# Optimization experiments

Measured on AMD Instinct MI355X. Metric: run time of the kernel, lower is better.

Reference implementation:

```python
import jax, jax.numpy as jnp
import numpy as np

R = 4  # num_relations


def rgcn_conv(x, src, dst, etype, W, root, bias):
    """PyG RGCNConv (aggr='mean', no self-loops):
    out_i = x_i @ root + bias + sum_r mean_{j in N_r(i)} (x_j @ W_r)
    x: [N,D], W: [R,D,H], root: [D,H], bias: [H]
    """
    N = x.shape[0]
    Rr, _, H = W.shape
    x_r = jnp.einsum('nd,rdh->rnh', x, W)          # [R,N,H] relation-transformed feats
    msg = x_r[etype, src]                          # [E,H] per-edge messages
    seg = etype * N + dst                          # combined (relation, dst) segment id
    sums = jax.ops.segment_sum(msg, seg, num_segments=Rr * N)            # [R*N,H]
    cnt = jax.ops.segment_sum(jnp.ones(msg.shape[0], msg.dtype), seg,
                              num_segments=Rr * N)                        # [R*N]
    mean = sums / jnp.maximum(cnt, 1.0)[:, None]
    agg = mean.reshape(Rr, N, H).sum(0)            # sum over relations
    return agg + x @ root + bias


def setup_inputs() -> dict:
    key = jax.random.key(0)
    ks = jax.random.split(key, 12)
    N, E, D, H, ED = 20000, 320000, 256, 256, 64
    s = lambda fan: 1.0 / np.sqrt(fan)
    return {
        'x': jax.random.normal(ks[0], (N, D), jnp.float32),
        'edge_index': jax.random.randint(ks[1], (2, E), 0, N),
        'edge_type': jax.random.randint(ks[2], (E,), 0, R),
        'edge_attr': jax.random.normal(ks[3], (E, ED), jnp.float32),
        'W0': jax.random.normal(ks[4], (R, D, H), jnp.float32) * s(D),
        'root0': jax.random.normal(ks[5], (D, H), jnp.float32) * s(D),
        'b0': jnp.zeros((H,), jnp.float32),
        'W1': jax.random.normal(ks[6], (R, H, H), jnp.float32) * s(H),
        'root1': jax.random.normal(ks[7], (H, H), jnp.float32) * s(H),
        'b1': jnp.zeros((H,), jnp.float32),
        'lin_w': jax.random.normal(ks[8], (H, 2), jnp.float32) * s(H),
        'lin_b': jnp.zeros((2,), jnp.float32),
    }


def reference(x, edge_index, edge_type, edge_attr, W0, root0, b0, W1, root1, b1, lin_w, lin_b):
    src, dst = edge_index[0], edge_index[1]
    h = jax.nn.relu(rgcn_conv(x, src, dst, edge_type, W0, root0, b0))
    h = rgcn_conv(h, src, dst, edge_type, W1, root1, b1)
    g = h.sum(axis=0, keepdims=True)   # global_add_pool, single graph -> [1,H]
    # dropout inactive in eval mode
    return g @ lin_w + lin_b           # [1,2]
```

## Files before the change

kernel.cpp:

```cpp
#include <hip/hip_runtime.h>
#include <hip/hip_bf16.h>

#define RREL 4
#define DIM 256
#define KDIM 1280
#define KMEAN 1024
#define BCAP 32

__device__ __forceinline__ float bf2f(unsigned short u) {
    union { unsigned int i; float f; } z; z.i = ((unsigned int)u) << 16; return z.f;
}
__device__ __forceinline__ unsigned short f2bf(float f) {
    __hip_bfloat16 h = __float2bfloat16(f);
    return *(unsigned short*)&h;
}

typedef __attribute__((ext_vector_type(8))) short bf16x8;
typedef __attribute__((ext_vector_type(8))) unsigned short u16x8;
typedef __attribute__((ext_vector_type(4))) float f32x4;


__global__ __launch_bounds__(256)
void prep(const int* __restrict__ etype, const int* __restrict__ src,
          const int* __restrict__ dst,
          int* __restrict__ counts, int* __restrict__ bucket, int N, int E,
          const float* __restrict__ x, __hip_bfloat16* __restrict__ xb, int n4,
          const float* __restrict__ W0, const float* __restrict__ root0,
          const float* __restrict__ W1, const float* __restrict__ root1,
          __hip_bfloat16* __restrict__ WT,
          int eb, int cb) {
    int b = blockIdx.x;
    if (b < eb) {
        int e = b * 256 + threadIdx.x;
        if (e < E) {
            int seg = etype[e] * N + dst[e];
            int p = atomicAdd(&counts[seg], 1);
            if (p < BCAP) bucket[(size_t)seg * BCAP + p] = src[e];
        }
    } else if (b < eb + cb) {
        int i = (b - eb) * 256 + threadIdx.x;
        if (i < n4) {
            float4 v = ((const float4*)x)[i];
            ushort4 u = make_ushort4(f2bf(v.x), f2bf(v.y), f2bf(v.z), f2bf(v.w));
            ((ushort4*)xb)[i] = u;
        }
    } else {
        __shared__ float tile[32][33];
        int q = b - eb - cb;
        int layer = q / 320; q -= layer * 320;
        int nblk = q / 40;
        int kblk = q - nblk * 40;
        const float* Wm = layer ? W1 : W0;
        const float* Rm = layer ? root1 : root0;
        int k0 = kblk * 32, n0 = nblk * 32;
        int tx = threadIdx.x & 31, ty = threadIdx.x >> 5;
        const float* srcp;
        int kbase;
        if (k0 < RREL * DIM) { srcp = Wm; kbase = k0; } else { srcp = Rm; kbase = k0 - RREL * DIM; }
#pragma unroll
        for (int j = 0; j < 4; j++) {
            int k = kbase + ty + j * 8;
            tile[ty + j * 8][tx] = srcp[(size_t)k * DIM + n0 + tx];
        }
        __syncthreads();
#pragma unroll
        for (int j = 0; j < 4; j++) {
            int n = n0 + ty + j * 8;
            WT[((size_t)layer * DIM + n) * KDIM + k0 + tx] = __float2bfloat16(tile[tx][ty + j * 8]);
        }
    }
}


__global__ __launch_bounds__(256)
void aggregate(const __hip_bfloat16* __restrict__ feat, const int* __restrict__ counts,
               const int* __restrict__ bucket, __hip_bfloat16* __restrict__ Y, int N) {
    int r = threadIdx.x >> 6, lane = threadIdx.x & 63;
    int h = lane >> 5, li = lane & 31;
    int i = blockIdx.x * 2 + h;
    if (i >= N) return;
    int seg = r * N + i;
    int cnt = min(counts[seg], BCAP);
    const unsigned short* fu = (const unsigned short*)feat;
    const int* bk = bucket + (size_t)seg * BCAP;
    float a[8] = {};
    for (int k = 0; k < cnt; k += 4) {
        int4 q = *(const int4*)(bk + k);
        float m1 = (k + 1 < cnt) ? 1.f : 0.f;
        float m2 = (k + 2 < cnt) ? 1.f : 0.f;
        float m3 = (k + 3 < cnt) ? 1.f : 0.f;
        int i0 = q.x;
        int i1 = m1 ? q.y : q.x;
        int i2 = m2 ? q.z : q.x;
        int i3 = m3 ? q.w : q.x;
        u16x8 v0 = *(const u16x8*)(fu + (size_t)i0 * DIM + li * 8);
        u16x8 v1 = *(const u16x8*)(fu + (size_t)i1 * DIM + li * 8);
        u16x8 v2 = *(const u16x8*)(fu + (size_t)i2 * DIM + li * 8);
        u16x8 v3 = *(const u16x8*)(fu + (size_t)i3 * DIM + li * 8);
#pragma unroll
        for (int j = 0; j < 8; j++)
            a[j] += bf2f(v0[j]) + m1 * bf2f(v1[j]) + m2 * bf2f(v2[j]) + m3 * bf2f(v3[j]);
    }
    float inv = (cnt > 0) ? 1.f / (float)cnt : 0.f;
    u16x8 u;
#pragma unroll
    for (int j = 0; j < 8; j++) u[j] = f2bf(a[j] * inv);
    *(u16x8*)((unsigned short*)Y + (size_t)i * KMEAN + r * DIM + li * 8) = u;
}


#define BMg 64
#define BKg 64

template <int MODE>
__global__ __launch_bounds__(256)
void gemm_mfma(const __hip_bfloat16* __restrict__ A,
               const __hip_bfloat16* __restrict__ Aself,
               const __hip_bfloat16* __restrict__ Bt,
               const float* __restrict__ bias,
               unsigned short* __restrict__ Cbf,
               float* __restrict__ gsum,
               int Nrows) {
    __shared__ short As[2][BMg * BKg];
    __shared__ short Bs[2][DIM * BKg];
    int t = threadIdx.x;
    int lane = t & 63;
    int w = t >> 6;
    size_t row0 = (size_t)blockIdx.x * BMg;

    const unsigned short* Ag = (const unsigned short*)A;
    const unsigned short* Sg = (const unsigned short*)Aself;
    const unsigned short* Bg = (const unsigned short*)Bt;

    float bb[4];
#pragma unroll
    for (int ni = 0; ni < 4; ni++) bb[ni] = bias[w * 64 + ni * 16 + (lane & 15)];

    f32x4 acc[4][4] = {};

    auto issue_tile = [&](int k0, short* as, short* bs) {
        const unsigned short* Abase;
        int kk, stride;
        if (k0 < KMEAN) { Abase = Ag; kk = k0; stride = KMEAN; }
        else            { Abase = Sg; kk = k0 - KMEAN; stride = DIM; }
#pragma unroll
        for (int h = 0; h < 2; h++) {
            int c = t + h * 256;
            int r = c >> 3, pl = c & 7, pg = pl ^ (r & 7);
            const unsigned short* ga = Abase + (row0 + r) * stride + kk + pg * 8;
            __builtin_amdgcn_global_load_lds(
                (const __attribute__((address_space(1))) void*)ga,
                (__attribute__((address_space(3))) void*)((char*)as + c * 16),
                16, 0, 0);
        }
#pragma unroll
        for (int h = 0; h < 8; h++) {
            int c = t + h * 256;
            int r = c >> 3, pl = c & 7, pg = pl ^ (r & 7);
            const unsigned short* gb = Bg + (size_t)r * KDIM + k0 + pg * 8;
            __builtin_amdgcn_global_load_lds(
                (const __attribute__((address_space(1))) void*)gb,
                (__attribute__((address_space(3))) void*)((char*)bs + c * 16),
                16, 0, 0);
        }
    };

    issue_tile(0, As[0], Bs[0]);
    int cur = 0;
    for (int k0 = 0; k0 < KDIM; k0 += BKg) {
        __syncthreads();
        if (k0 + BKg < KDIM) issue_tile(k0 + BKg, As[cur ^ 1], Bs[cur ^ 1]);
        const short* as = As[cur];
        const short* bs = Bs[cur];
#pragma unroll
        for (int ks = 0; ks < 2; ks++) {
            int p = ks * 4 + (lane >> 4);
            bf16x8 af[4], bfr[4];
#pragma unroll
            for (int mi = 0; mi < 4; mi++) {
                int m = mi * 16 + (lane & 15);
                af[mi] = *(const bf16x8*)&as[m * 64 + (p ^ (m & 7)) * 8];
            }
#pragma unroll
            for (int ni = 0; ni < 4; ni++) {
                int n = w * 64 + ni * 16 + (lane & 15);
                bfr[ni] = *(const bf16x8*)&bs[n * 64 + (p ^ (n & 7)) * 8];
            }
#pragma unroll
            for (int mi = 0; mi < 4; mi++)
#pragma unroll
                for (int ni = 0; ni < 4; ni++)
                    acc[mi][ni] = __builtin_amdgcn_mfma_f32_16x16x32_bf16(af[mi], bfr[ni], acc[mi][ni], 0, 0, 0);
        }
        cur ^= 1;
    }

    if (MODE == 0) {
#pragma unroll
        for (int mi = 0; mi < 4; mi++) {
#pragma unroll
            for (int j = 0; j < 4; j++) {
                size_t row = row0 + mi * 16 + (lane >> 4) * 4 + j;
                if (row < (size_t)Nrows) {
#pragma unroll
                    for (int ni = 0; ni < 4; ni++) {
                        size_t col = w * 64 + ni * 16 + (lane & 15);
                        float v = fmaxf(acc[mi][ni][j] + bb[ni], 0.f);
                        Cbf[row * DIM + col] = f2bf(v);
                    }
                }
            }
        }
    } else {
        float cs[4] = {};
#pragma unroll
        for (int ni = 0; ni < 4; ni++) {
#pragma unroll
            for (int mi = 0; mi < 4; mi++)
#pragma unroll
                for (int j = 0; j < 4; j++) {
                    size_t row = row0 + mi * 16 + (lane >> 4) * 4 + j;
                    if (row < (size_t)Nrows) cs[ni] += acc[mi][ni][j] + bb[ni];
                }
            cs[ni] += __shfl_xor(cs[ni], 16, 64);
            cs[ni] += __shfl_xor(cs[ni], 32, 64);
        }
        if (lane < 16) {
#pragma unroll
            for (int ni = 0; ni < 4; ni++)
                atomicAdd(&gsum[w * 64 + ni * 16 + lane], cs[ni]);
        }
    }
}


__global__ void final_lin(const float* __restrict__ g, const float* __restrict__ lw,
                          const float* __restrict__ lb, float* __restrict__ out) {
    __shared__ float s0[256], s1[256];
    int t = threadIdx.x;
    float gv = g[t];
    s0[t] = gv * lw[t * 2 + 0];
    s1[t] = gv * lw[t * 2 + 1];
    __syncthreads();
    for (int off = 128; off > 0; off >>= 1) {
        if (t < off) { s0[t] += s0[t + off]; s1[t] += s1[t + off]; }
        __syncthreads();
    }
    if (t == 0) { out[0] = s0[0] + lb[0]; out[1] = s1[0] + lb[1]; }
}


static inline char* align_up(char* p, size_t a) {
    return (char*)(((uintptr_t)p + (a - 1)) & ~(uintptr_t)(a - 1));
}

extern "C" void kernel_launch(void* const* d_in, const int* in_sizes, int n_in,
                              void* d_out, int out_size, void* d_ws, size_t ws_size,
                              hipStream_t stream) {
    const float* x     = (const float*)d_in[0];
    const int*   eidx  = (const int*)d_in[1];
    const int*   etype = (const int*)d_in[2];
    const float* W0    = (const float*)d_in[4];
    const float* root0 = (const float*)d_in[5];
    const float* b0    = (const float*)d_in[6];
    const float* W1    = (const float*)d_in[7];
    const float* root1 = (const float*)d_in[8];
    const float* b1    = (const float*)d_in[9];
    const float* lin_w = (const float*)d_in[10];
    const float* lin_b = (const float*)d_in[11];
    float* out = (float*)d_out;

    const int N = in_sizes[0] / DIM;
    const int E = in_sizes[2];
    const int RN = RREL * N;
    const int* src = eidx;
    const int* dst = eidx + E;

    const int gx = (N + BMg - 1) / BMg;
    const int Mpad = gx * BMg;

    char* w = (char*)d_ws;
    int* counts  = (int*)w; w += (size_t)RN * 4;
    float* g     = (float*)w; w += 256 * 4;
    size_t zero_bytes = (size_t)RN * 4 + 1024;
    int* bucket  = (int*)w; w += (size_t)RN * BCAP * 4;
    w = align_up(w, 16);
    __hip_bfloat16* WT = (__hip_bfloat16*)w; w += (size_t)2 * DIM * KDIM * 2;
    w = align_up(w, 16);
    __hip_bfloat16* Y  = (__hip_bfloat16*)w; w += (size_t)Mpad * KMEAN * 2;
    __hip_bfloat16* xb = (__hip_bfloat16*)w; w += (size_t)Mpad * DIM * 2;
    __hip_bfloat16* h1 = (__hip_bfloat16*)w; w += (size_t)Mpad * DIM * 2;

    hipMemsetAsync(counts, 0, zero_bytes, stream);

    int eb = (E + 255) / 256;
    int n4 = N * DIM / 4;
    int cb = (n4 + 255) / 256;
    int wb = (KDIM / 32) * (DIM / 32) * 2;

    prep<<<eb + cb + wb, 256, 0, stream>>>(etype, src, dst, counts, bucket, N, E,
                                           x, xb, n4,
                                           W0, root0, W1, root1, WT, eb, cb);

    int ab = (N + 1) / 2;
    aggregate<<<ab, 256, 0, stream>>>(xb, counts, bucket, Y, N);
    gemm_mfma<0><<<gx, 256, 0, stream>>>(Y, xb, WT, b0, (unsigned short*)h1, nullptr, N);
    aggregate<<<ab, 256, 0, stream>>>(h1, counts, bucket, Y, N);
    gemm_mfma<1><<<gx, 256, 0, stream>>>(Y, h1, WT + (size_t)DIM * KDIM, b1, nullptr, g, N);

    final_lin<<<1, 256, 0, stream>>>(g, lin_w, lin_b, out);
}
```

Measured before the change: 273.4 us.

## Collapse second RGCN layer into weighted column sums plus a GEMV

Because the second layer output is only sum-pooled, the layer is linear in h1. The sum over nodes can therefore be rewritten as per-source weighted column sums of h1, with weights 1/cnt accumulated per edge and relation, followed by a small GEMV with W1 and root1. This drops the second aggregation pass and the second big GEMM, as well as the W1 transpose and convert. It adds an edge-wise atomic scatter into wsr and float atomics in the column-sum kernel, which changes summation order. It also computes the second layer in fp32 from bf16 h1, and it uses the uncapped counts for the weights, whereas the kept aggregation path truncates buckets at BCAP.

Measured after the change: 270.6 us. No clear change (-1.0%).

```diff
diff --git a/kernel.cpp b/kernel.cpp
--- a/kernel.cpp
+++ b/kernel.cpp
@@ -18,6 +18,7 @@
 typedef __attribute__((ext_vector_type(8))) short bf16x8;
 typedef __attribute__((ext_vector_type(8))) unsigned short u16x8;
 typedef __attribute__((ext_vector_type(4))) float f32x4;
+typedef __attribute__((ext_vector_type(4))) float fx4;
 
 
 __global__ __launch_bounds__(256)
@@ -26,7 +27,6 @@
           int* __restrict__ counts, int* __restrict__ bucket, int N, int E,
           const float* __restrict__ x, __hip_bfloat16* __restrict__ xb, int n4,
           const float* __restrict__ W0, const float* __restrict__ root0,
-          const float* __restrict__ W1, const float* __restrict__ root1,
           __hip_bfloat16* __restrict__ WT,
           int eb, int cb) {
     int b = blockIdx.x;
@@ -40,23 +40,20 @@
     } else if (b < eb + cb) {
         int i = (b - eb) * 256 + threadIdx.x;
         if (i < n4) {
-            float4 v = ((const float4*)x)[i];
+            fx4 v = *((const fx4*)x + i);
             ushort4 u = make_ushort4(f2bf(v.x), f2bf(v.y), f2bf(v.z), f2bf(v.w));
             ((ushort4*)xb)[i] = u;
         }
     } else {
         __shared__ float tile[32][33];
         int q = b - eb - cb;
-        int layer = q / 320; q -= layer * 320;
         int nblk = q / 40;
         int kblk = q - nblk * 40;
-        const float* Wm = layer ? W1 : W0;
-        const float* Rm = layer ? root1 : root0;
         int k0 = kblk * 32, n0 = nblk * 32;
         int tx = threadIdx.x & 31, ty = threadIdx.x >> 5;
         const float* srcp;
         int kbase;
-        if (k0 < RREL * DIM) { srcp = Wm; kbase = k0; } else { srcp = Rm; kbase = k0 - RREL * DIM; }
+        if (k0 < RREL * DIM) { srcp = W0; kbase = k0; } else { srcp = root0; kbase = k0 - RREL * DIM; }
 #pragma unroll
         for (int j = 0; j < 4; j++) {
             int k = kbase + ty + j * 8;
@@ -66,7 +63,7 @@
 #pragma unroll
         for (int j = 0; j < 4; j++) {
             int n = n0 + ty + j * 8;
-            WT[((size_t)layer * DIM + n) * KDIM + k0 + tx] = __float2bfloat16(tile[tx][ty + j * 8]);
+            WT[(size_t)n * KDIM + k0 + tx] = __float2bfloat16(tile[tx][ty + j * 8]);
         }
     }
 }
@@ -74,7 +71,19 @@
 
 __global__ __launch_bounds__(256)
 void aggregate(const __hip_bfloat16* __restrict__ feat, const int* __restrict__ counts,
-               const int* __restrict__ bucket, __hip_bfloat16* __restrict__ Y, int N) {
+               const int* __restrict__ bucket, __hip_bfloat16* __restrict__ Y, int N,
+               const int* __restrict__ etype, const int* __restrict__ srcv,
+               const int* __restrict__ dstv, float* __restrict__ wsr, int E, int ab) {
+    if ((int)blockIdx.x >= ab) {
+        int e = (blockIdx.x - ab) * 256 + threadIdx.x;
+        if (e < E) {
+            int r = etype[e];
+            int seg = r * N + dstv[e];
+            float sc = 1.f / (float)counts[seg];
+            atomicAdd(&wsr[(size_t)srcv[e] * RREL + r], sc);
+        }
+        return;
+    }
     int r = threadIdx.x >> 6, lane = threadIdx.x & 63;
     int h = lane >> 5, li = lane & 31;
     int i = blockIdx.x * 2 + h;
@@ -112,14 +121,12 @@
 #define BMg 64
 #define BKg 64
 
-template <int MODE>
 __global__ __launch_bounds__(256)
 void gemm_mfma(const __hip_bfloat16* __restrict__ A,
                const __hip_bfloat16* __restrict__ Aself,
                const __hip_bfloat16* __restrict__ Bt,
                const float* __restrict__ bias,
                unsigned short* __restrict__ Cbf,
-               float* __restrict__ gsum,
                int Nrows) {
     __shared__ short As[2][BMg * BKg];
     __shared__ short Bs[2][DIM * BKg];
@@ -195,42 +202,62 @@
         cur ^= 1;
     }
 
-    if (MODE == 0) {
-#pragma unroll
-        for (int mi = 0; mi < 4; mi++) {
-#pragma unroll
-            for (int j = 0; j < 4; j++) {
-                size_t row = row0 + mi * 16 + (lane >> 4) * 4 + j;
-                if (row < (size_t)Nrows) {
-#pragma unroll
-                    for (int ni = 0; ni < 4; ni++) {
-                        size_t col = w * 64 + ni * 16 + (lane & 15);
-                        float v = fmaxf(acc[mi][ni][j] + bb[ni], 0.f);
-                        Cbf[row * DIM + col] = f2bf(v);
-                    }
+#pragma unroll
+    for (int mi = 0; mi < 4; mi++) {
+#pragma unroll
+        for (int j = 0; j < 4; j++) {
+            size_t row = row0 + mi * 16 + (lane >> 4) * 4 + j;
+            if (row < (size_t)Nrows) {
+#pragma unroll
+                for (int ni = 0; ni < 4; ni++) {
+                    size_t col = w * 64 + ni * 16 + (lane & 15);
+                    float v = fmaxf(acc[mi][ni][j] + bb[ni], 0.f);
+                    Cbf[row * DIM + col] = f2bf(v);
                 }
             }
         }
-    } else {
-        float cs[4] = {};
-#pragma unroll
-        for (int ni = 0; ni < 4; ni++) {
-#pragma unroll
-            for (int mi = 0; mi < 4; mi++)
-#pragma unroll
-                for (int j = 0; j < 4; j++) {
-                    size_t row = row0 + mi * 16 + (lane >> 4) * 4 + j;
-                    if (row < (size_t)Nrows) cs[ni] += acc[mi][ni][j] + bb[ni];
-                }
-            cs[ni] += __shfl_xor(cs[ni], 16, 64);
-            cs[ni] += __shfl_xor(cs[ni], 32, 64);
-        }
-        if (lane < 16) {
-#pragma unroll
-            for (int ni = 0; ni < 4; ni++)
-                atomicAdd(&gsum[w * 64 + ni * 16 + lane], cs[ni]);
-        }
-    }
+    }
+}
+
+
+__global__ __launch_bounds__(256)
+void wcolsum(const unsigned short* __restrict__ h1, const float* __restrict__ wsr,
+             int N, float* __restrict__ sv) {
+    int t = threadIdx.x;
+    int i0 = blockIdx.x * 256;
+    int iend = min(i0 + 256, N);
+    float a0 = 0.f, a1 = 0.f, a2 = 0.f, a3 = 0.f, as = 0.f;
+#pragma unroll 4
+    for (int i = i0; i < iend; i++) {
+        float v = bf2f(h1[(size_t)i * DIM + t]);
+        fx4 wv = *(const fx4*)(wsr + (size_t)i * RREL);
+        as += v;
+        a0 += wv.x * v; a1 += wv.y * v; a2 += wv.z * v; a3 += wv.w * v;
+    }
+    atomicAdd(&sv[0 * DIM + t], a0);
+    atomicAdd(&sv[1 * DIM + t], a1);
+    atomicAdd(&sv[2 * DIM + t], a2);
+    atomicAdd(&sv[3 * DIM + t], a3);
+    atomicAdd(&sv[4 * DIM + t], as);
+}
+
+
+__global__ __launch_bounds__(256)
+void gemv(const float* __restrict__ sv, const float* __restrict__ W1,
+          const float* __restrict__ root1, const float* __restrict__ b1,
+          int N, float* __restrict__ g) {
+    int t = threadIdx.x;
+    int kk0 = blockIdx.x * 64;
+    float acc = 0.f;
+    for (int kk = kk0; kk < kk0 + 64; kk++) {
+        int r = kk >> 8;
+        int k = kk & 255;
+        const float* row = (r < RREL) ? (W1 + ((size_t)r * DIM + k) * DIM)
+                                      : (root1 + (size_t)k * DIM);
+        acc += sv[kk] * row[t];
+    }
+    if (blockIdx.x == 0) acc += (float)N * b1[t];
+    atomicAdd(&g[t], acc);
 }
 
 
@@ -280,12 +307,14 @@
     const int Mpad = gx * BMg;
 
     char* w = (char*)d_ws;
-    int* counts  = (int*)w; w += (size_t)RN * 4;
-    float* g     = (float*)w; w += 256 * 4;
-    size_t zero_bytes = (size_t)RN * 4 + 1024;
-    int* bucket  = (int*)w; w += (size_t)RN * BCAP * 4;
+    int*   counts = (int*)w;   w += (size_t)RN * 4;
+    float* wsr    = (float*)w; w += (size_t)N * RREL * 4;
+    float* sv     = (float*)w; w += (size_t)5 * DIM * 4;
+    float* g      = (float*)w; w += 256 * 4;
+    size_t zero_bytes = (size_t)RN * 4 + (size_t)N * RREL * 4 + 5 * DIM * 4 + 256 * 4;
+    int* bucket = (int*)w; w += (size_t)RN * BCAP * 4;
     w = align_up(w, 16);
-    __hip_bfloat16* WT = (__hip_bfloat16*)w; w += (size_t)2 * DIM * KDIM * 2;
+    __hip_bfloat16* WT = (__hip_bfloat16*)w; w += (size_t)DIM * KDIM * 2;
     w = align_up(w, 16);
     __hip_bfloat16* Y  = (__hip_bfloat16*)w; w += (size_t)Mpad * KMEAN * 2;
     __hip_bfloat16* xb = (__hip_bfloat16*)w; w += (size_t)Mpad * DIM * 2;
@@ -296,17 +325,17 @@
     int eb = (E + 255) / 256;
     int n4 = N * DIM / 4;
     int cb = (n4 + 255) / 256;
-    int wb = (KDIM / 32) * (DIM / 32) * 2;
+    int wb = (KDIM / 32) * (DIM / 32);
 
     prep<<<eb + cb + wb, 256, 0, stream>>>(etype, src, dst, counts, bucket, N, E,
-                                           x, xb, n4,
-                                           W0, root0, W1, root1, WT, eb, cb);
+                                           x, xb, n4, W0, root0, WT, eb, cb);
 
     int ab = (N + 1) / 2;
-    aggregate<<<ab, 256, 0, stream>>>(xb, counts, bucket, Y, N);
-    gemm_mfma<0><<<gx, 256, 0, stream>>>(Y, xb, WT, b0, (unsigned short*)h1, nullptr, N);
-    aggregate<<<ab, 256, 0, stream>>>(h1, counts, bucket, Y, N);
-    gemm_mfma<1><<<gx, 256, 0, stream>>>(Y, h1, WT + (size_t)DIM * KDIM, b1, nullptr, g, N);
+    aggregate<<<ab + eb, 256, 0, stream>>>(xb, counts, bucket, Y, N,
+                                           etype, src, dst, wsr, E, ab);
+    gemm_mfma<<<gx, 256, 0, stream>>>(Y, xb, WT, b0, (unsigned short*)h1, N);
+    wcolsum<<<(N + 255) / 256, 256, 0, stream>>>((const unsigned short*)h1, wsr, N, sv);
+    gemv<<<KDIM / 64, 256, 0, stream>>>(sv, W1, root1, b1, N, g);
 
     final_lin<<<1, 256, 0, stream>>>(g, lin_w, lin_b, out);
 }
```
